# Kernel tuning notes

Measured on AMD Instinct MI355X. Metric: run time of the kernel, lower is better.

Reference implementation:

```python
import jax, jax.numpy as jnp
import numpy as np

D = 768
N_HEADS = 12
D_HEAD = D // N_HEADS


def setup_inputs() -> dict:
    key = jax.random.key(0)
    ks = jax.random.split(key, 7)
    sequences = jax.random.normal(ks[0], (32, 512, D), dtype=jnp.float32)
    s = 1.0 / np.sqrt(D_HEAD)
    Wq = jax.random.uniform(ks[1], (N_HEADS, D_HEAD, D_HEAD), jnp.float32, -s, s)
    Wk = jax.random.uniform(ks[2], (N_HEADS, D_HEAD, D_HEAD), jnp.float32, -s, s)
    Wv = jax.random.uniform(ks[3], (N_HEADS, D_HEAD, D_HEAD), jnp.float32, -s, s)
    bq = jax.random.uniform(ks[4], (N_HEADS, D_HEAD), jnp.float32, -s, s)
    bk = jax.random.uniform(ks[5], (N_HEADS, D_HEAD), jnp.float32, -s, s)
    bv = jax.random.uniform(ks[6], (N_HEADS, D_HEAD), jnp.float32, -s, s)
    return {"sequences": sequences, "Wq": Wq, "Wk": Wk, "Wv": Wv,
            "bq": bq, "bk": bk, "bv": bv}


def reference(sequences, Wq, Wk, Wv, bq, bk, bv):
    b, s, d = sequences.shape
    # split channels into heads: [b, s, h, d_head]
    x = sequences.reshape(b, s, N_HEADS, D_HEAD)
    # per-head linear (block-diagonal QKV); Linear: y = x @ W^T + b
    q = jnp.einsum('bshd,hed->bshe', x, Wq) + bq
    k = jnp.einsum('bshd,hed->bshe', x, Wk) + bk
    v = jnp.einsum('bshd,hed->bshe', x, Wv) + bv
    # NOTE: original module does NOT scale by 1/sqrt(d_head)
    scores = jnp.einsum('bshe,bthe->bhst', q, k)  # [b, h, s, s]
    attn = jax.nn.softmax(scores, axis=-1)
    out = jnp.einsum('bhst,bthe->bshe', attn, v)  # [b, s, h, d_head]
    return out.reshape(b, s, d)
```

## Files before the change

### kernel.cpp

```cpp
#include <hip/hip_runtime.h>
#include <stdint.h>

#define B_ 32
#define S_ 512
#define D_ 768
#define H_ 12
#define DH_ 64

typedef __attribute__((ext_vector_type(8))) short bf16x8;
typedef __attribute__((ext_vector_type(4))) float f32x4;
typedef __attribute__((ext_vector_type(4))) short short4v;
typedef __attribute__((ext_vector_type(4))) unsigned int u32x4;

#define WP 72
#define VP 136
#define KC_U 0
#define VT_U 9216
#define WS_U 0
#define XS_U 17920
#define SMEM_BYTES 54272

__device__ __forceinline__ unsigned short f2bf(float f) {
  uint32_t u = __builtin_bit_cast(uint32_t, f);
  return (unsigned short)((u + 0x7fffu + ((u >> 16) & 1u)) >> 16);
}

__device__ __forceinline__ uint32_t pk2bf(float a, float b) {
  uint32_t ua = __builtin_bit_cast(uint32_t, a) + 0x8000u;
  uint32_t ub = __builtin_bit_cast(uint32_t, b) + 0x8000u;
  return __builtin_amdgcn_perm(ub, ua, 0x07060302u);
}

__device__ __forceinline__ int sigma(int tile, int r16) {
  return 32 * (tile >> 1) + 8 * (r16 >> 2) + 4 * (tile & 1) + (r16 & 3);
}

__device__ __forceinline__ bf16x8 ldfrag8(const unsigned short* p) {
  return *(const bf16x8*)p;
}

#define MFMA(a, b, c) __builtin_amdgcn_mfma_f32_16x16x32_bf16((a), (b), (c), 0, 0, 0)

extern "C" __global__ void __launch_bounds__(512, 2)
mhsa_mfma(const float* __restrict__ seq, const float* __restrict__ Wq,
          const float* __restrict__ Wk, const float* __restrict__ Wv,
          const float* __restrict__ bq, const float* __restrict__ bk,
          const float* __restrict__ bv, float* __restrict__ out)
{
  extern __shared__ unsigned short lds[];
  unsigned short* Ws = lds + WS_U;
  unsigned short* xs = lds + XS_U;
  unsigned short* Kc = lds + KC_U;
  unsigned short* Vt = lds + VT_U;

  const int tid = threadIdx.x;
  const int lane = tid & 63;
  const int w = tid >> 6;
  const int g = lane >> 4;
  const int r16 = lane & 15;
  const int bh = blockIdx.x;
  const int b = bh / H_;
  const int h = bh - b * H_;
  const int r0 = blockIdx.y * 256;
  const int cb8 = 8 * g;

  const float* seqh = seq + (size_t)b * (S_ * D_) + h * DH_;

  #pragma unroll
  for (int i = 0; i < 24; ++i) {
    int idx = tid + i * 512;
    int row = idx >> 6, col = idx & 63;
    const float* src = (idx < 4096) ? (Wq + h * 4096 + idx)
                     : (idx < 8192) ? (Wk + h * 4096 + (idx - 4096))
                                    : (Wv + h * 4096 + (idx - 8192));
    Ws[row * WP + col] = f2bf(*src);
  }
  __syncthreads();

  bf16x8 wkB[4][2];
  #pragma unroll
  for (int e4 = 0; e4 < 4; ++e4)
    #pragma unroll
    for (int ec = 0; ec < 2; ++ec)
      wkB[e4][ec] = ldfrag8(Ws + (64 + 16 * e4 + r16) * WP + 32 * ec + cb8);
  const int ev = w & 3;
  const int th = w >> 2;
  bf16x8 wvA[2];
  #pragma unroll
  for (int ec = 0; ec < 2; ++ec)
    wvA[ec] = ldfrag8(Ws + (128 + 16 * ev + r16) * WP + 32 * ec + cb8);

  float bk_l[4], bv_l[4];
  #pragma unroll
  for (int e4 = 0; e4 < 4; ++e4) bk_l[e4] = bk[h * 64 + 16 * e4 + r16];
  #pragma unroll
  for (int rr = 0; rr < 4; ++rr) bv_l[rr] = bv[h * 64 + 16 * ev + 4 * g + rr];

  bf16x8 qB[2][2];
  for (int cq = 0; cq < 2; ++cq) {
    __syncthreads();
    #pragma unroll
    for (int i = 0; i < 4; ++i) {
      int idx = tid + i * 512;
      int row = idx >> 4, c4 = (idx & 15) << 2;
      const float4 xv = *(const float4*)(seqh + (size_t)(r0 + cq * 128 + row) * D_ + c4);
      uint2 p;
      p.x = pk2bf(xv.x, xv.y);
      p.y = pk2bf(xv.z, xv.w);
      *(uint2*)(xs + row * WP + c4) = p;
    }
    __syncthreads();
    if (th == cq) {
      const int lr = 32 * ev;
      #pragma unroll
      for (int mt = 0; mt < 2; ++mt) {
        bf16x8 xB[2];
        #pragma unroll
        for (int ec = 0; ec < 2; ++ec)
          xB[ec] = ldfrag8(xs + (lr + 16 * mt + r16) * WP + 32 * ec + cb8);
        f32x4 qt[4];
        #pragma unroll
        for (int e4 = 0; e4 < 4; ++e4) {
          f32x4 acc = {0.f, 0.f, 0.f, 0.f};
          #pragma unroll
          for (int ec = 0; ec < 2; ++ec)
            acc = MFMA(ldfrag8(Ws + (16 * e4 + r16) * WP + 32 * ec + cb8), xB[ec], acc);
          qt[e4] = acc;
        }
        #pragma unroll
        for (int ec2 = 0; ec2 < 2; ++ec2) {
          const int eA = 2 * ec2, eB = 2 * ec2 + 1;
          u32x4 t;
          t[0] = pk2bf(qt[eA][0] + bq[h * 64 + 16 * eA + 4 * g + 0],
                       qt[eA][1] + bq[h * 64 + 16 * eA + 4 * g + 1]);
          t[1] = pk2bf(qt[eA][2] + bq[h * 64 + 16 * eA + 4 * g + 2],
                       qt[eA][3] + bq[h * 64 + 16 * eA + 4 * g + 3]);
          t[2] = pk2bf(qt[eB][0] + bq[h * 64 + 16 * eB + 4 * g + 0],
                       qt[eB][1] + bq[h * 64 + 16 * eB + 4 * g + 1]);
          t[3] = pk2bf(qt[eB][2] + bq[h * 64 + 16 * eB + 4 * g + 2],
                       qt[eB][3] + bq[h * 64 + 16 * eB + 4 * g + 3]);
          qB[mt][ec2] = __builtin_bit_cast(bf16x8, t);
        }
      }
    }
  }

  f32x4 O[2][4];
  #pragma unroll
  for (int mt = 0; mt < 2; ++mt)
    #pragma unroll
    for (int e4 = 0; e4 < 4; ++e4) O[mt][e4] = {0.f, 0.f, 0.f, 0.f};
  float m_st[2] = {-1e30f, -1e30f}, l_st[2] = {0.f, 0.f};
  const int m0w = w * 32;

  for (int c = 0; c < 4; ++c) {
    __syncthreads();
    #pragma unroll
    for (int i = 0; i < 4; ++i) {
      int idx = tid + i * 512;
      int row = idx >> 4, c4 = (idx & 15) << 2;
      const float4 xv = *(const float4*)(seqh + (size_t)(c * 128 + row) * D_ + c4);
      uint2 p;
      p.x = pk2bf(xv.x, xv.y);
      p.y = pk2bf(xv.z, xv.w);
      *(uint2*)(xs + row * WP + c4) = p;
    }
    __syncthreads();

    {
      bf16x8 aX[2];
      #pragma unroll
      for (int ec = 0; ec < 2; ++ec)
        aX[ec] = ldfrag8(xs + (w * 16 + r16) * WP + 32 * ec + cb8);
      #pragma unroll
      for (int e4 = 0; e4 < 4; ++e4) {
        f32x4 acc = {0.f, 0.f, 0.f, 0.f};
        #pragma unroll
        for (int ec = 0; ec < 2; ++ec) acc = MFMA(aX[ec], wkB[e4][ec], acc);
        const float bkv = bk_l[e4];
        const int rb = w * 16 + 4 * g;
        const int cs = sigma(e4, r16);
        uint32_t k01 = pk2bf(acc[0] + bkv, acc[1] + bkv);
        uint32_t k23 = pk2bf(acc[2] + bkv, acc[3] + bkv);
        Kc[(rb + 0) * WP + cs] = (unsigned short)k01;
        Kc[(rb + 1) * WP + cs] = (unsigned short)(k01 >> 16);
        Kc[(rb + 2) * WP + cs] = (unsigned short)k23;
        Kc[(rb + 3) * WP + cs] = (unsigned short)(k23 >> 16);
      }
    }
    #pragma unroll
    for (int ttl = 0; ttl < 4; ++ttl) {
      int tt = th * 4 + ttl;
      bf16x8 xB[2];
      #pragma unroll
      for (int ec = 0; ec < 2; ++ec)
        xB[ec] = ldfrag8(xs + (tt * 16 + r16) * WP + 32 * ec + cb8);
      f32x4 acc = {0.f, 0.f, 0.f, 0.f};
      #pragma unroll
      for (int ec = 0; ec < 2; ++ec) acc = MFMA(wvA[ec], xB[ec], acc);
      const int rb = 16 * ev + 4 * g;
      const int cs = sigma(tt, r16);
      uint32_t v01 = pk2bf(acc[0] + bv_l[0], acc[1] + bv_l[1]);
      uint32_t v23 = pk2bf(acc[2] + bv_l[2], acc[3] + bv_l[3]);
      Vt[(rb + 0) * VP + cs] = (unsigned short)v01;
      Vt[(rb + 1) * VP + cs] = (unsigned short)(v01 >> 16);
      Vt[(rb + 2) * VP + cs] = (unsigned short)v23;
      Vt[(rb + 3) * VP + cs] = (unsigned short)(v23 >> 16);
    }
    __syncthreads();

    bf16x8 pA[4][2];
    #pragma unroll
    for (int mt = 0; mt < 2; ++mt) {
      f32x4 st[8];
      #pragma unroll
      for (int tt = 0; tt < 8; ++tt) {
        bf16x8 aK[2];
        #pragma unroll
        for (int ec = 0; ec < 2; ++ec)
          aK[ec] = ldfrag8(Kc + (tt * 16 + r16) * WP + 32 * ec + cb8);
        f32x4 acc = {0.f, 0.f, 0.f, 0.f};
        #pragma unroll
        for (int ec = 0; ec < 2; ++ec) acc = MFMA(aK[ec], qB[mt][ec], acc);
        st[tt] = acc;
      }
      float mx = st[0][0];
      #pragma unroll
      for (int tt = 0; tt < 8; ++tt)
        #pragma unroll
        for (int rr = 0; rr < 4; ++rr) mx = fmaxf(mx, st[tt][rr]);
      mx = fmaxf(mx, __shfl_xor(mx, 16, 64));
      mx = fmaxf(mx, __shfl_xor(mx, 32, 64));
      if (!__all(mx <= m_st[mt] + 8.0f)) {
        float mn = fmaxf(m_st[mt], mx);
        float al = __expf(m_st[mt] - mn);
        m_st[mt] = mn;
        float af[4];
        #pragma unroll
        for (int rr = 0; rr < 4; ++rr) af[rr] = __shfl(al, 4 * g + rr, 64);
        #pragma unroll
        for (int e4 = 0; e4 < 4; ++e4)
          #pragma unroll
          for (int rr = 0; rr < 4; ++rr) O[mt][e4][rr] *= af[rr];
        l_st[mt] *= al;
      }
      const float mcur = m_st[mt];
      float sum = 0.f;
      #pragma unroll
      for (int tt = 0; tt < 8; ++tt)
        #pragma unroll
        for (int rr = 0; rr < 4; ++rr) {
          float pv = __expf(st[tt][rr] - mcur);
          st[tt][rr] = pv;
          sum += pv;
        }
      sum += __shfl_xor(sum, 16, 64);
      sum += __shfl_xor(sum, 32, 64);
      l_st[mt] += sum;
      #pragma unroll
      for (int u = 0; u < 4; ++u) {
        u32x4 t;
        t[0] = pk2bf(st[2 * u][0], st[2 * u][1]);
        t[1] = pk2bf(st[2 * u][2], st[2 * u][3]);
        t[2] = pk2bf(st[2 * u + 1][0], st[2 * u + 1][1]);
        t[3] = pk2bf(st[2 * u + 1][2], st[2 * u + 1][3]);
        pA[u][mt] = __builtin_bit_cast(bf16x8, t);
      }
    }
    #pragma unroll
    for (int u = 0; u < 4; ++u) {
      bf16x8 vB[4];
      #pragma unroll
      for (int e4 = 0; e4 < 4; ++e4)
        vB[e4] = ldfrag8(Vt + (16 * e4 + r16) * VP + 32 * u + cb8);
      #pragma unroll
      for (int mt = 0; mt < 2; ++mt)
        #pragma unroll
        for (int e4 = 0; e4 < 4; ++e4)
          O[mt][e4] = MFMA(pA[u][mt], vB[e4], O[mt][e4]);
    }
  }

  #pragma unroll
  for (int mt = 0; mt < 2; ++mt) {
    float inv[4];
    #pragma unroll
    for (int rr = 0; rr < 4; ++rr) inv[rr] = 1.0f / __shfl(l_st[mt], 4 * g + rr, 64);
    #pragma unroll
    for (int e4 = 0; e4 < 4; ++e4)
      #pragma unroll
      for (int rr = 0; rr < 4; ++rr)
        out[(size_t)(b * S_ + r0 + m0w + 16 * mt + 4 * g + rr) * D_ + h * DH_ + 16 * e4 + r16] =
            O[mt][e4][rr] * inv[rr];
  }
}

extern "C" void kernel_launch(void* const* d_in, const int* in_sizes, int n_in,
                              void* d_out, int out_size, void* d_ws, size_t ws_size,
                              hipStream_t stream) {
  const float* seq = (const float*)d_in[0];
  const float* Wq  = (const float*)d_in[1];
  const float* Wk  = (const float*)d_in[2];
  const float* Wv  = (const float*)d_in[3];
  const float* bq  = (const float*)d_in[4];
  const float* bk  = (const float*)d_in[5];
  const float* bv  = (const float*)d_in[6];
  float* outp = (float*)d_out;

  hipFuncSetAttribute((const void*)mhsa_mfma,
                      hipFuncAttributeMaxDynamicSharedMemorySize, SMEM_BYTES);
  dim3 grid(B_ * H_, 2);
  mhsa_mfma<<<grid, 512, SMEM_BYTES, stream>>>(seq, Wq, Wk, Wv, bq, bk, bv, outp);
}
```

Measured before the change: 81.63 us.

## Split fused attention into projection kernel plus double-buffered attention kernel

Splits the single fused kernel into two. A projection kernel computes bf16 Q, K and V once per (batch, head) and writes them to workspace, with Q stored in MFMA fragment order. An attention kernel then streams K/V in 64-row double-buffered LDS chunks at higher occupancy. Before, each of the two row-halves recomputed the full K/V projection for its (batch, head); that redundancy is removed. The cost is a global round-trip of bf16 Q/K/V and an extra launch. It falls back to the fused kernel when the workspace is too small.

Result: faster. 79.33 us (-2.8%).

```diff
diff --git a/kernel.cpp b/kernel.cpp
--- a/kernel.cpp
+++ b/kernel.cpp
@@ -14,33 +14,322 @@
 
 #define WP 72
 #define VP 136
-#define KC_U 0
-#define VT_U 9216
-#define WS_U 0
-#define XS_U 17920
-#define SMEM_BYTES 54272
+
+#define QOFF 0
+#define KOFF 12582912
+#define VOFF 25165824
+#define WS_NEED 75497472ULL
 
 __device__ __forceinline__ unsigned short f2bf(float f) {
   uint32_t u = __builtin_bit_cast(uint32_t, f);
   return (unsigned short)((u + 0x7fffu + ((u >> 16) & 1u)) >> 16);
 }
-
 __device__ __forceinline__ uint32_t pk2bf(float a, float b) {
   uint32_t ua = __builtin_bit_cast(uint32_t, a) + 0x8000u;
   uint32_t ub = __builtin_bit_cast(uint32_t, b) + 0x8000u;
   return __builtin_amdgcn_perm(ub, ua, 0x07060302u);
 }
-
 __device__ __forceinline__ int sigma(int tile, int r16) {
   return 32 * (tile >> 1) + 8 * (r16 >> 2) + 4 * (tile & 1) + (r16 & 3);
 }
-
 __device__ __forceinline__ bf16x8 ldfrag8(const unsigned short* p) {
   return *(const bf16x8*)p;
 }
-
 #define MFMA(a, b, c) __builtin_amdgcn_mfma_f32_16x16x32_bf16((a), (b), (c), 0, 0, 0)
 
+#define P_SMEM 81920
+extern "C" __global__ void __launch_bounds__(512, 2)
+proj_kernel(const float* __restrict__ seq, const float* __restrict__ Wq,
+            const float* __restrict__ Wk, const float* __restrict__ Wv,
+            const float* __restrict__ bq, const float* __restrict__ bk,
+            const float* __restrict__ bv, unsigned short* __restrict__ ws)
+{
+  extern __shared__ unsigned short lds[];
+  unsigned short* Ws   = lds;
+  unsigned short* xs   = lds + 13824;
+  unsigned short* Kimg = lds + 23040;
+  unsigned short* Vimg = lds + 32256;
+
+  const int tid = threadIdx.x;
+  const int lane = tid & 63;
+  const int w = tid >> 6;
+  const int g = lane >> 4;
+  const int r16 = lane & 15;
+  const int cb8 = 8 * g;
+  const int bh = blockIdx.x;
+  const int h = bh - (bh / H_) * H_;
+  const int b = bh / H_;
+  const int tbase = blockIdx.y * 256;
+
+  const float* seqh = seq + (size_t)b * (S_ * D_) + h * DH_;
+
+  #pragma unroll
+  for (int i = 0; i < 24; ++i) {
+    int idx = tid + i * 512;
+    int row = idx >> 6, col = idx & 63;
+    const float* src = (idx < 4096) ? (Wq + h * 4096 + idx)
+                     : (idx < 8192) ? (Wk + h * 4096 + (idx - 4096))
+                                    : (Wv + h * 4096 + (idx - 8192));
+    Ws[row * WP + col] = f2bf(*src);
+  }
+  __syncthreads();
+
+  bf16x8 wkB[4][2];
+  #pragma unroll
+  for (int e4 = 0; e4 < 4; ++e4)
+    #pragma unroll
+    for (int ec = 0; ec < 2; ++ec)
+      wkB[e4][ec] = ldfrag8(Ws + (64 + 16 * e4 + r16) * WP + 32 * ec + cb8);
+  const int ev = w & 3;
+  const int th = w >> 2;
+  bf16x8 wvA[2];
+  #pragma unroll
+  for (int ec = 0; ec < 2; ++ec)
+    wvA[ec] = ldfrag8(Ws + (128 + 16 * ev + r16) * WP + 32 * ec + cb8);
+
+  float bk_l[4], bv_l[4];
+  #pragma unroll
+  for (int e4 = 0; e4 < 4; ++e4) bk_l[e4] = bk[h * 64 + 16 * e4 + r16];
+  #pragma unroll
+  for (int rr = 0; rr < 4; ++rr) bv_l[rr] = bv[h * 64 + 16 * ev + 4 * g + rr];
+
+  for (int c = 0; c < 2; ++c) {
+    const int rowb = tbase + c * 128;
+    #pragma unroll
+    for (int i = 0; i < 4; ++i) {
+      int idx = tid + i * 512;
+      int row = idx >> 4, c4 = (idx & 15) << 2;
+      const float4 xv = *(const float4*)(seqh + (size_t)(rowb + row) * D_ + c4);
+      uint2 p;
+      p.x = pk2bf(xv.x, xv.y);
+      p.y = pk2bf(xv.z, xv.w);
+      *(uint2*)(xs + row * WP + c4) = p;
+    }
+    __syncthreads();
+
+    {
+      bf16x8 xB[2];
+      #pragma unroll
+      for (int ec = 0; ec < 2; ++ec)
+        xB[ec] = ldfrag8(xs + (16 * w + r16) * WP + 32 * ec + cb8);
+      f32x4 qt[4];
+      #pragma unroll
+      for (int e4 = 0; e4 < 4; ++e4) {
+        f32x4 acc = {0.f, 0.f, 0.f, 0.f};
+        #pragma unroll
+        for (int ec = 0; ec < 2; ++ec)
+          acc = MFMA(ldfrag8(Ws + (16 * e4 + r16) * WP + 32 * ec + cb8), xB[ec], acc);
+        qt[e4] = acc;
+      }
+      const int tile = blockIdx.y * 16 + c * 8 + w;
+      #pragma unroll
+      for (int ec2 = 0; ec2 < 2; ++ec2) {
+        const int eA = 2 * ec2, eB = 2 * ec2 + 1;
+        u32x4 t;
+        t[0] = pk2bf(qt[eA][0] + bq[h * 64 + 16 * eA + 4 * g + 0],
+                     qt[eA][1] + bq[h * 64 + 16 * eA + 4 * g + 1]);
+        t[1] = pk2bf(qt[eA][2] + bq[h * 64 + 16 * eA + 4 * g + 2],
+                     qt[eA][3] + bq[h * 64 + 16 * eA + 4 * g + 3]);
+        t[2] = pk2bf(qt[eB][0] + bq[h * 64 + 16 * eB + 4 * g + 0],
+                     qt[eB][1] + bq[h * 64 + 16 * eB + 4 * g + 1]);
+        t[3] = pk2bf(qt[eB][2] + bq[h * 64 + 16 * eB + 4 * g + 2],
+                     qt[eB][3] + bq[h * 64 + 16 * eB + 4 * g + 3]);
+        *(u32x4*)(ws + QOFF + (size_t)(((bh * 32 + tile) * 2 + ec2) * 512 + lane * 8)) = t;
+      }
+    }
+    {
+      bf16x8 aX[2];
+      #pragma unroll
+      for (int ec = 0; ec < 2; ++ec)
+        aX[ec] = ldfrag8(xs + (w * 16 + r16) * WP + 32 * ec + cb8);
+      #pragma unroll
+      for (int e4 = 0; e4 < 4; ++e4) {
+        f32x4 acc = {0.f, 0.f, 0.f, 0.f};
+        #pragma unroll
+        for (int ec = 0; ec < 2; ++ec) acc = MFMA(aX[ec], wkB[e4][ec], acc);
+        const float bkv = bk_l[e4];
+        const int rb = w * 16 + 4 * g;
+        const int cs = sigma(e4, r16);
+        uint32_t k01 = pk2bf(acc[0] + bkv, acc[1] + bkv);
+        uint32_t k23 = pk2bf(acc[2] + bkv, acc[3] + bkv);
+        Kimg[(rb + 0) * WP + cs] = (unsigned short)k01;
+        Kimg[(rb + 1) * WP + cs] = (unsigned short)(k01 >> 16);
+        Kimg[(rb + 2) * WP + cs] = (unsigned short)k23;
+        Kimg[(rb + 3) * WP + cs] = (unsigned short)(k23 >> 16);
+      }
+    }
+    #pragma unroll
+    for (int ttl = 0; ttl < 4; ++ttl) {
+      int tt = th * 4 + ttl;
+      bf16x8 xB[2];
+      #pragma unroll
+      for (int ec = 0; ec < 2; ++ec)
+        xB[ec] = ldfrag8(xs + (tt * 16 + r16) * WP + 32 * ec + cb8);
+      f32x4 acc = {0.f, 0.f, 0.f, 0.f};
+      #pragma unroll
+      for (int ec = 0; ec < 2; ++ec) acc = MFMA(wvA[ec], xB[ec], acc);
+      const int rb = 16 * ev + 4 * g;
+      const int cs = sigma(tt, r16);
+      uint32_t v01 = pk2bf(acc[0] + bv_l[0], acc[1] + bv_l[1]);
+      uint32_t v23 = pk2bf(acc[2] + bv_l[2], acc[3] + bv_l[3]);
+      Vimg[(rb + 0) * VP + cs] = (unsigned short)v01;
+      Vimg[(rb + 1) * VP + cs] = (unsigned short)(v01 >> 16);
+      Vimg[(rb + 2) * VP + cs] = (unsigned short)v23;
+      Vimg[(rb + 3) * VP + cs] = (unsigned short)(v23 >> 16);
+    }
+    __syncthreads();
+    #pragma unroll
+    for (int ii = 0; ii < 2; ++ii) {
+      int idx = tid + ii * 512;
+      int row = idx >> 3, seg = idx & 7;
+      uint4 kv = *(const uint4*)(Kimg + row * WP + seg * 8);
+      *(uint4*)(ws + KOFF + (size_t)((bh * 512 + rowb + row) * 64 + seg * 8)) = kv;
+    }
+    #pragma unroll
+    for (int ii = 0; ii < 2; ++ii) {
+      int idx = tid + ii * 512;
+      int e = idx >> 4, seg2 = idx & 15;
+      uint4 vv = *(const uint4*)(Vimg + e * VP + seg2 * 8);
+      *(uint4*)(ws + VOFF + (size_t)((bh * 64 + e) * 512 + rowb + seg2 * 8)) = vv;
+    }
+    __syncthreads();
+  }
+}
+
+#define A_SMEM 36864
+extern "C" __global__ void __launch_bounds__(512, 6)
+attn_kernel(const unsigned short* __restrict__ ws, float* __restrict__ out)
+{
+  extern __shared__ unsigned short alds[];
+  const int tid = threadIdx.x;
+  const int lane = tid & 63;
+  const int w = tid >> 6;
+  const int g = lane >> 4;
+  const int r16 = lane & 15;
+  const int cb8 = 8 * g;
+  const int bh = blockIdx.x;
+  const int b = bh / H_;
+  const int h = bh - b * H_;
+  const int by = blockIdx.y;
+  const int r0 = by * 256;
+
+  bf16x8 qB[2][2];
+  #pragma unroll
+  for (int mt = 0; mt < 2; ++mt)
+    #pragma unroll
+    for (int ec = 0; ec < 2; ++ec)
+      qB[mt][ec] = *(const bf16x8*)(ws + QOFF +
+          (size_t)(((bh * 32 + 16 * by + 2 * w + mt) * 2 + ec) * 512 + lane * 8));
+
+  const int srow = tid >> 3, sseg = (tid & 7) * 8;
+  const size_t kbase = (size_t)(bh * 512 + srow) * 64 + sseg;
+  const size_t vbase = (size_t)(bh * 64 + srow) * 512 + sseg;
+  {
+    uint4 kv = *(const uint4*)(ws + KOFF + kbase);
+    *(uint4*)(alds + 0 + srow * WP + sseg) = kv;
+    uint4 vv = *(const uint4*)(ws + VOFF + vbase);
+    *(uint4*)(alds + 9216 + srow * WP + sseg) = vv;
+  }
+  __syncthreads();
+
+  f32x4 O[2][4];
+  #pragma unroll
+  for (int mt = 0; mt < 2; ++mt)
+    #pragma unroll
+    for (int e4 = 0; e4 < 4; ++e4) O[mt][e4] = {0.f, 0.f, 0.f, 0.f};
+  float m_st[2] = {-1e30f, -1e30f}, l_st[2] = {0.f, 0.f};
+
+  for (int c = 0; c < 8; ++c) {
+    const int us = c & 1;
+    const unsigned short* Kcur = alds + (us ? 4608 : 0);
+    const unsigned short* Vcur = alds + 9216 + (us ? 4608 : 0);
+    if (c < 7) {
+      unsigned short* Knxt = alds + (us ? 0 : 4608);
+      unsigned short* Vnxt = alds + 9216 + (us ? 0 : 4608);
+      uint4 kv = *(const uint4*)(ws + KOFF + kbase + (size_t)(c + 1) * 64 * 64);
+      *(uint4*)(Knxt + srow * WP + sseg) = kv;
+      uint4 vv = *(const uint4*)(ws + VOFF + vbase + (size_t)(c + 1) * 64);
+      *(uint4*)(Vnxt + srow * WP + sseg) = vv;
+    }
+    #pragma unroll
+    for (int mt = 0; mt < 2; ++mt) {
+      f32x4 st[4];
+      #pragma unroll
+      for (int tt = 0; tt < 4; ++tt) {
+        f32x4 acc = {0.f, 0.f, 0.f, 0.f};
+        #pragma unroll
+        for (int ec = 0; ec < 2; ++ec)
+          acc = MFMA(ldfrag8(Kcur + (tt * 16 + r16) * WP + 32 * ec + cb8), qB[mt][ec], acc);
+        st[tt] = acc;
+      }
+      float mx = st[0][0];
+      #pragma unroll
+      for (int tt = 0; tt < 4; ++tt)
+        #pragma unroll
+        for (int rr = 0; rr < 4; ++rr) mx = fmaxf(mx, st[tt][rr]);
+      mx = fmaxf(mx, __shfl_xor(mx, 16, 64));
+      mx = fmaxf(mx, __shfl_xor(mx, 32, 64));
+      if (!__all(mx <= m_st[mt] + 8.0f)) {
+        float mn = fmaxf(m_st[mt], mx);
+        float al = __expf(m_st[mt] - mn);
+        m_st[mt] = mn;
+        float af[4];
+        #pragma unroll
+        for (int rr = 0; rr < 4; ++rr) af[rr] = __shfl(al, 4 * g + rr, 64);
+        #pragma unroll
+        for (int e4 = 0; e4 < 4; ++e4)
+          #pragma unroll
+          for (int rr = 0; rr < 4; ++rr) O[mt][e4][rr] *= af[rr];
+        l_st[mt] *= al;
+      }
+      const float mcur = m_st[mt];
+      float sum = 0.f;
+      #pragma unroll
+      for (int tt = 0; tt < 4; ++tt)
+        #pragma unroll
+        for (int rr = 0; rr < 4; ++rr) {
+          float pv = __expf(st[tt][rr] - mcur);
+          st[tt][rr] = pv;
+          sum += pv;
+        }
+      sum += __shfl_xor(sum, 16, 64);
+      sum += __shfl_xor(sum, 32, 64);
+      l_st[mt] += sum;
+      #pragma unroll
+      for (int u = 0; u < 2; ++u) {
+        u32x4 t;
+        t[0] = pk2bf(st[2 * u][0], st[2 * u][1]);
+        t[1] = pk2bf(st[2 * u][2], st[2 * u][3]);
+        t[2] = pk2bf(st[2 * u + 1][0], st[2 * u + 1][1]);
+        t[3] = pk2bf(st[2 * u + 1][2], st[2 * u + 1][3]);
+        bf16x8 f = __builtin_bit_cast(bf16x8, t);
+        #pragma unroll
+        for (int e4 = 0; e4 < 4; ++e4) {
+          bf16x8 vB = ldfrag8(Vcur + (16 * e4 + r16) * WP + 32 * u + cb8);
+          O[mt][e4] = MFMA(f, vB, O[mt][e4]);
+        }
+      }
+    }
+    __syncthreads();
+  }
+
+  #pragma unroll
+  for (int mt = 0; mt < 2; ++mt) {
+    float inv[4];
+    #pragma unroll
+    for (int rr = 0; rr < 4; ++rr) inv[rr] = 1.0f / __shfl(l_st[mt], 4 * g + rr, 64);
+    #pragma unroll
+    for (int e4 = 0; e4 < 4; ++e4)
+      #pragma unroll
+      for (int rr = 0; rr < 4; ++rr)
+        out[(size_t)(b * S_ + r0 + w * 32 + 16 * mt + 4 * g + rr) * D_ + h * DH_ + 16 * e4 + r16] =
+            O[mt][e4][rr] * inv[rr];
+  }
+}
+
+#define FWP 72
+#define FVP 136
+#define F_SMEM 54272
 extern "C" __global__ void __launch_bounds__(512, 2)
 mhsa_mfma(const float* __restrict__ seq, const float* __restrict__ Wq,
           const float* __restrict__ Wk, const float* __restrict__ Wv,
@@ -48,10 +337,10 @@
           const float* __restrict__ bv, float* __restrict__ out)
 {
   extern __shared__ unsigned short lds[];
-  unsigned short* Ws = lds + WS_U;
-  unsigned short* xs = lds + XS_U;
-  unsigned short* Kc = lds + KC_U;
-  unsigned short* Vt = lds + VT_U;
+  unsigned short* Ws = lds;
+  unsigned short* xs = lds + 17920;
+  unsigned short* Kc = lds;
+  unsigned short* Vt = lds + 9216;
 
   const int tid = threadIdx.x;
   const int lane = tid & 63;
@@ -73,7 +362,7 @@
     const float* src = (idx < 4096) ? (Wq + h * 4096 + idx)
                      : (idx < 8192) ? (Wk + h * 4096 + (idx - 4096))
                                     : (Wv + h * 4096 + (idx - 8192));
-    Ws[row * WP + col] = f2bf(*src);
+    Ws[row * FWP + col] = f2bf(*src);
   }
   __syncthreads();
 
@@ -82,13 +371,13 @@
   for (int e4 = 0; e4 < 4; ++e4)
     #pragma unroll
     for (int ec = 0; ec < 2; ++ec)
-      wkB[e4][ec] = ldfrag8(Ws + (64 + 16 * e4 + r16) * WP + 32 * ec + cb8);
+      wkB[e4][ec] = ldfrag8(Ws + (64 + 16 * e4 + r16) * FWP + 32 * ec + cb8);
   const int ev = w & 3;
   const int th = w >> 2;
   bf16x8 wvA[2];
   #pragma unroll
   for (int ec = 0; ec < 2; ++ec)
-    wvA[ec] = ldfrag8(Ws + (128 + 16 * ev + r16) * WP + 32 * ec + cb8);
+    wvA[ec] = ldfrag8(Ws + (128 + 16 * ev + r16) * FWP + 32 * ec + cb8);
 
   float bk_l[4], bv_l[4];
   #pragma unroll
@@ -107,7 +396,7 @@
       uint2 p;
       p.x = pk2bf(xv.x, xv.y);
       p.y = pk2bf(xv.z, xv.w);
-      *(uint2*)(xs + row * WP + c4) = p;
+      *(uint2*)(xs + row * FWP + c4) = p;
     }
     __syncthreads();
     if (th == cq) {
@@ -117,14 +406,14 @@
         bf16x8 xB[2];
         #pragma unroll
         for (int ec = 0; ec < 2; ++ec)
-          xB[ec] = ldfrag8(xs + (lr + 16 * mt + r16) * WP + 32 * ec + cb8);
+          xB[ec] = ldfrag8(xs + (lr + 16 * mt + r16) * FWP + 32 * ec + cb8);
         f32x4 qt[4];
         #pragma unroll
         for (int e4 = 0; e4 < 4; ++e4) {
           f32x4 acc = {0.f, 0.f, 0.f, 0.f};
           #pragma unroll
           for (int ec = 0; ec < 2; ++ec)
-            acc = MFMA(ldfrag8(Ws + (16 * e4 + r16) * WP + 32 * ec + cb8), xB[ec], acc);
+            acc = MFMA(ldfrag8(Ws + (16 * e4 + r16) * FWP + 32 * ec + cb8), xB[ec], acc);
           qt[e4] = acc;
         }
         #pragma unroll
@@ -163,15 +452,14 @@
       uint2 p;
       p.x = pk2bf(xv.x, xv.y);
       p.y = pk2bf(xv.z, xv.w);
-      *(uint2*)(xs + row * WP + c4) = p;
-    }
-    __syncthreads();
-
+      *(uint2*)(xs + row * FWP + c4) = p;
+    }
+    __syncthreads();
     {
       bf16x8 aX[2];
       #pragma unroll
       for (int ec = 0; ec < 2; ++ec)
-        aX[ec] = ldfrag8(xs + (w * 16 + r16) * WP + 32 * ec + cb8);
+        aX[ec] = ldfrag8(xs + (w * 16 + r16) * FWP + 32 * ec + cb8);
       #pragma unroll
       for (int e4 = 0; e4 < 4; ++e4) {
         f32x4 acc = {0.f, 0.f, 0.f, 0.f};
@@ -182,10 +470,10 @@
         const int cs = sigma(e4, r16);
         uint32_t k01 = pk2bf(acc[0] + bkv, acc[1] + bkv);
         uint32_t k23 = pk2bf(acc[2] + bkv, acc[3] + bkv);
-        Kc[(rb + 0) * WP + cs] = (unsigned short)k01;
-        Kc[(rb + 1) * WP + cs] = (unsigned short)(k01 >> 16);
-        Kc[(rb + 2) * WP + cs] = (unsigned short)k23;
-        Kc[(rb + 3) * WP + cs] = (unsigned short)(k23 >> 16);
+        Kc[(rb + 0) * FWP + cs] = (unsigned short)k01;
+        Kc[(rb + 1) * FWP + cs] = (unsigned short)(k01 >> 16);
+        Kc[(rb + 2) * FWP + cs] = (unsigned short)k23;
+        Kc[(rb + 3) * FWP + cs] = (unsigned short)(k23 >> 16);
       }
     }
     #pragma unroll
@@ -194,7 +482,7 @@
       bf16x8 xB[2];
       #pragma unroll
       for (int ec = 0; ec < 2; ++ec)
-        xB[ec] = ldfrag8(xs + (tt * 16 + r16) * WP + 32 * ec + cb8);
+        xB[ec] = ldfrag8(xs + (tt * 16 + r16) * FWP + 32 * ec + cb8);
       f32x4 acc = {0.f, 0.f, 0.f, 0.f};
       #pragma unroll
       for (int ec = 0; ec < 2; ++ec) acc = MFMA(wvA[ec], xB[ec], acc);
@@ -202,10 +490,10 @@
       const int cs = sigma(tt, r16);
       uint32_t v01 = pk2bf(acc[0] + bv_l[0], acc[1] + bv_l[1]);
       uint32_t v23 = pk2bf(acc[2] + bv_l[2], acc[3] + bv_l[3]);
-      Vt[(rb + 0) * VP + cs] = (unsigned short)v01;
-      Vt[(rb + 1) * VP + cs] = (unsigned short)(v01 >> 16);
-      Vt[(rb + 2) * VP + cs] = (unsigned short)v23;
-      Vt[(rb + 3) * VP + cs] = (unsigned short)(v23 >> 16);
+      Vt[(rb + 0) * FVP + cs] = (unsigned short)v01;
+      Vt[(rb + 1) * FVP + cs] = (unsigned short)(v01 >> 16);
+      Vt[(rb + 2) * FVP + cs] = (unsigned short)v23;
+      Vt[(rb + 3) * FVP + cs] = (unsigned short)(v23 >> 16);
     }
     __syncthreads();
 
@@ -218,7 +506,7 @@
         bf16x8 aK[2];
         #pragma unroll
         for (int ec = 0; ec < 2; ++ec)
-          aK[ec] = ldfrag8(Kc + (tt * 16 + r16) * WP + 32 * ec + cb8);
+          aK[ec] = ldfrag8(Kc + (tt * 16 + r16) * FWP + 32 * ec + cb8);
         f32x4 acc = {0.f, 0.f, 0.f, 0.f};
         #pragma unroll
         for (int ec = 0; ec < 2; ++ec) acc = MFMA(aK[ec], qB[mt][ec], acc);
@@ -272,7 +560,7 @@
       bf16x8 vB[4];
       #pragma unroll
       for (int e4 = 0; e4 < 4; ++e4)
-        vB[e4] = ldfrag8(Vt + (16 * e4 + r16) * VP + 32 * u + cb8);
+        vB[e4] = ldfrag8(Vt + (16 * e4 + r16) * FVP + 32 * u + cb8);
       #pragma unroll
       for (int mt = 0; mt < 2; ++mt)
         #pragma unroll
@@ -307,8 +595,19 @@
   const float* bv  = (const float*)d_in[6];
   float* outp = (float*)d_out;
 
-  hipFuncSetAttribute((const void*)mhsa_mfma,
-                      hipFuncAttributeMaxDynamicSharedMemorySize, SMEM_BYTES);
-  dim3 grid(B_ * H_, 2);
-  mhsa_mfma<<<grid, 512, SMEM_BYTES, stream>>>(seq, Wq, Wk, Wv, bq, bk, bv, outp);
-}
+  if (ws_size >= WS_NEED) {
+    unsigned short* ws = (unsigned short*)d_ws;
+    hipFuncSetAttribute((const void*)proj_kernel,
+                        hipFuncAttributeMaxDynamicSharedMemorySize, P_SMEM);
+    hipFuncSetAttribute((const void*)attn_kernel,
+                        hipFuncAttributeMaxDynamicSharedMemorySize, A_SMEM);
+    dim3 grid(B_ * H_, 2);
+    proj_kernel<<<grid, 512, P_SMEM, stream>>>(seq, Wq, Wk, Wv, bq, bk, bv, ws);
+    attn_kernel<<<grid, 512, A_SMEM, stream>>>(ws, outp);
+  } else {
+    hipFuncSetAttribute((const void*)mhsa_mfma,
+                        hipFuncAttributeMaxDynamicSharedMemorySize, F_SMEM);
+    dim3 grid(B_ * H_, 2);
+    mhsa_mfma<<<grid, 512, F_SMEM, stream>>>(seq, Wq, Wk, Wv, bq, bk, bv, outp);
+  }
+}
```
